# Performance work log

Hardware: AMD Instinct MI355X
Metric: run time of the kernel (lower is better)

## Reference

```python
import jax, jax.numpy as jnp
import numpy as np

B = 64        # number of queries (eg_idx groups)
EPQ = 2048    # edges per query (contiguous blocks, sorted by eg_idx)
E = B * EPQ   # 131072 total edges
D = 128       # n_dims_in; G3 dim = 4*D = 512
N = 50000     # number of visited nodes
K = 256       # max_edges (top-k per query)


def setup_inputs() -> dict:
    key = jax.random.key(0)
    ks = jax.random.split(key, 9)
    scale = np.sqrt(2.0 / (4 * D)).astype(np.float32)
    return {
        "visited_node_score": jax.random.uniform(ks[0], (N,), jnp.float32),
        "visited_node_representation": jax.random.normal(ks[1], (N, D), jnp.float32),
        "rel_emb": jax.random.normal(ks[2], (E, D), jnp.float32),
        "query_src_ts_emb": jax.random.normal(ks[3], (B, D), jnp.float32),
        "query_rel_emb": jax.random.normal(ks[4], (B, D), jnp.float32),
        "Wq": jax.random.normal(ks[5], (4 * D, 4 * D), jnp.float32) * scale,
        "Wk": jax.random.normal(ks[6], (4 * D, 4 * D), jnp.float32) * scale,
        # sorted eg_idx with exactly EPQ edges per query -> regular per-group topk
        "eg_idx": (jnp.arange(E) // EPQ).astype(jnp.int32),
        "node_idx_i": jax.random.randint(ks[7], (E,), 0, N, jnp.int32),
        "node_idx_j": jax.random.randint(ks[8], (E,), 0, N, jnp.int32),
        "k": K,
    }


def segment_softmax(logits, seg, num_segments):
    # numerically-stable softmax over edges sharing the same source node
    m = jax.ops.segment_max(logits, seg, num_segments=num_segments)
    m = jax.lax.stop_gradient(m)
    ex = jnp.exp(logits - m[seg])
    s = jax.ops.segment_sum(ex, seg, num_segments=num_segments)
    return ex / s[seg]


def reference(visited_node_score, visited_node_representation, rel_emb,
              query_src_ts_emb, query_rel_emb, Wq, Wk,
              eg_idx, node_idx_i, node_idx_j, k):
    # gather node / query embeddings per edge (torch index_select)
    hvi = visited_node_representation[node_idx_i]          # [E, D]
    hvj = visited_node_representation[node_idx_j]          # [E, D]
    qs = query_src_ts_emb[eg_idx]                          # [E, D]
    qr = query_rel_emb[eg_idx]                             # [E, D]
    # G3 bilinear: sum(query_proj(cat(left)) * key_proj(cat(right)), -1)
    left = jnp.concatenate([hvi, rel_emb, qs, qr], axis=-1)   # [E, 4D]
    right = jnp.concatenate([hvj, rel_emb, qs, qr], axis=-1)  # [E, 4D]
    logits = jnp.sum((left @ Wq.T) * (right @ Wk.T), axis=-1) # [E]
    # softmax over edges grouped by source node idx (edges[:, -2])
    attn = segment_softmax(logits, node_idx_i, N)              # [E]
    src_score = visited_node_score[node_idx_i]                 # [E]
    target_score = attn * src_score                            # [E]
    # per-query top-k pruning (each query owns a contiguous EPQ block, EPQ > k)
    top_vals, top_idx = jax.lax.top_k(target_score.reshape(B, EPQ), k)
    flat_idx = (top_idx + jnp.arange(B, dtype=top_idx.dtype)[:, None] * EPQ).reshape(-1)
    pruned_attn = attn[flat_idx]                # transition_logits_pruned_softmax
    pruned_src = src_score[flat_idx]            # pruned_src_score
    pruned_tgt = node_idx_j[flat_idx]           # pruned_edges[:, 7]
    # 'sum' node score aggregation: sparse mm == segment_sum of attn * src_score
    updated_node_score = jax.ops.segment_sum(pruned_attn * pruned_src,
                                             pruned_tgt, num_segments=N)
    return updated_node_score
```

## Files before the change

kernel.cpp:

```cpp
#include <hip/hip_runtime.h>
#include <cstddef>

#define EPQ_SHIFT 11
#define KSEL 256

typedef __attribute__((ext_vector_type(8))) short short8v;
typedef __attribute__((ext_vector_type(4))) float float4v;

__device__ __forceinline__ unsigned enc_f(float f) {
  unsigned u = __float_as_uint(f);
  return (u & 0x80000000u) ? ~u : (u | 0x80000000u);
}
__device__ __forceinline__ float dec_f(unsigned k) {
  unsigned u = (k & 0x80000000u) ? (k ^ 0x80000000u) : ~k;
  return __uint_as_float(u);
}
__device__ __forceinline__ unsigned short f2bf(float x) {
  unsigned u = __float_as_uint(x);
  return (unsigned short)((u + 0x7FFFu + ((u >> 16) & 1u)) >> 16);
}

__global__ __launch_bounds__(256) void k1_gemmM(
    const float* __restrict__ Wq, const float* __restrict__ Wk,
    float* __restrict__ M, float* __restrict__ Mt,
    unsigned short* __restrict__ Mh, unsigned short* __restrict__ Ml,
    unsigned short* __restrict__ Mth, unsigned short* __restrict__ Mtl,
    float* __restrict__ outz, float* __restrict__ segsum,
    unsigned* __restrict__ segkey, int N) {
  int tid = threadIdx.x;
  {
    int bid = blockIdx.y * gridDim.x + blockIdx.x;
    for (int idx = bid * 256 + tid; idx < N; idx += 16384) {
      outz[idx] = 0.f;
      segsum[idx] = 0.f;
      segkey[idx] = 0u;
    }
  }
  __shared__ float as[16][64];
  __shared__ float bs[16][64];
  int tx = tid & 15, ty = tid >> 4;
  int c1b = blockIdx.y * 64, c2b = blockIdx.x * 64;
  float acc[4][4] = {};
  for (int k0 = 0; k0 < 512; k0 += 16) {
#pragma unroll
    for (int l = 0; l < 4; ++l) {
      int lin = tid + l * 256;
      int kk = lin >> 6, c = lin & 63;
      as[kk][c] = Wq[(k0 + kk) * 512 + c1b + c];
      bs[kk][c] = Wk[(k0 + kk) * 512 + c2b + c];
    }
    __syncthreads();
#pragma unroll
    for (int kk = 0; kk < 16; ++kk) {
      float a[4], b[4];
#pragma unroll
      for (int m = 0; m < 4; ++m) a[m] = as[kk][ty * 4 + m];
#pragma unroll
      for (int n = 0; n < 4; ++n) b[n] = bs[kk][tx * 4 + n];
#pragma unroll
      for (int m = 0; m < 4; ++m)
#pragma unroll
        for (int n = 0; n < 4; ++n) acc[m][n] += a[m] * b[n];
    }
    __syncthreads();
  }
#pragma unroll
  for (int m = 0; m < 4; ++m)
#pragma unroll
    for (int n = 0; n < 4; ++n) {
      int c1 = c1b + ty * 4 + m, c2 = c2b + tx * 4 + n;
      float v = acc[m][n];
      M[c1 * 512 + c2] = v;
      Mt[c2 * 512 + c1] = v;
      unsigned short h = f2bf(v);
      unsigned short lo = f2bf(v - __uint_as_float((unsigned)h << 16));
      Mh[c1 * 512 + c2] = h;
      Ml[c1 * 512 + c2] = lo;
      Mth[c2 * 512 + c1] = h;
      Mtl[c2 * 512 + c1] = lo;
    }
}

#define STAGE_A_F32(SRC_PTR)                                                 \
  {                                                                          \
    const float* s = (SRC_PTR);                                              \
    float4 v0 = *(const float4*)&s[0];                                       \
    float4 v1 = *(const float4*)&s[4];                                       \
    float4 v2 = *(const float4*)&s[8];                                       \
    float4 v3 = *(const float4*)&s[12];                                      \
    float vv[16] = {v0.x, v0.y, v0.z, v0.w, v1.x, v1.y, v1.z, v1.w,          \
                    v2.x, v2.y, v2.z, v2.w, v3.x, v3.y, v3.z, v3.w};         \
    unsigned hw[8], lw[8];                                                   \
    _Pragma("unroll") for (int j = 0; j < 8; ++j) {                          \
      unsigned short h0 = f2bf(vv[2 * j]);                                   \
      unsigned short h1 = f2bf(vv[2 * j + 1]);                               \
      unsigned short l0 =                                                    \
          f2bf(vv[2 * j] - __uint_as_float((unsigned)h0 << 16));             \
      unsigned short l1 =                                                    \
          f2bf(vv[2 * j + 1] - __uint_as_float((unsigned)h1 << 16));         \
      hw[j] = (unsigned)h0 | ((unsigned)h1 << 16);                           \
      lw[j] = (unsigned)l0 | ((unsigned)l1 << 16);                           \
    }                                                                        \
    int sw = (sn >> 1) & 3;                                                  \
    int g0 = (shalf * 2) ^ sw, g1 = (shalf * 2 + 1) ^ sw;                    \
    *(uint4*)&Ah[sn][g0 * 8] = make_uint4(hw[0], hw[1], hw[2], hw[3]);       \
    *(uint4*)&Ah[sn][g1 * 8] = make_uint4(hw[4], hw[5], hw[6], hw[7]);       \
    *(uint4*)&Al[sn][g0 * 8] = make_uint4(lw[0], lw[1], lw[2], lw[3]);       \
    *(uint4*)&Al[sn][g1 * 8] = make_uint4(lw[4], lw[5], lw[6], lw[7]);       \
  }

#define STAGE_B_BF16(HSRC, LSRC)                                             \
  {                                                                          \
    const unsigned short* sh_ = (HSRC);                                      \
    const unsigned short* sl_ = (LSRC);                                      \
    uint4 q0 = *(const uint4*)&sh_[0];                                       \
    uint4 q1 = *(const uint4*)&sh_[8];                                       \
    uint4 p0 = *(const uint4*)&sl_[0];                                       \
    uint4 p1 = *(const uint4*)&sl_[8];                                       \
    int sw = (sn >> 1) & 3;                                                  \
    int g0 = (shalf * 2) ^ sw, g1 = (shalf * 2 + 1) ^ sw;                    \
    *(uint4*)&Bh[sn][g0 * 8] = q0;                                           \
    *(uint4*)&Bh[sn][g1 * 8] = q1;                                           \
    *(uint4*)&Bl[sn][g0 * 8] = p0;                                           \
    *(uint4*)&Bl[sn][g1 * 8] = p1;                                           \
  }

#define MFMA_CHUNK()                                                         \
  {                                                                          \
    int ln = lane & 15, kq = lane >> 4;                                      \
    short8v ah[4], al[4];                                                    \
    _Pragma("unroll") for (int r = 0; r < 4; ++r) {                          \
      int row = wr2 * 64 + r * 16 + ln;                                      \
      int gg = kq ^ ((row >> 1) & 3);                                        \
      ah[r] = *(const short8v*)&Ah[row][gg * 8];                             \
      al[r] = *(const short8v*)&Al[row][gg * 8];                             \
    }                                                                        \
    _Pragma("unroll") for (int c = 0; c < 4; ++c) {                          \
      int col = wc2 * 64 + c * 16 + ln;                                      \
      int gg = kq ^ ((col >> 1) & 3);                                        \
      short8v bh = *(const short8v*)&Bh[col][gg * 8];                        \
      short8v bl = *(const short8v*)&Bl[col][gg * 8];                        \
      _Pragma("unroll") for (int r = 0; r < 4; ++r) {                        \
        acc[r][c] = __builtin_amdgcn_mfma_f32_16x16x32_bf16(                 \
            ah[r], bh, acc[r][c], 0, 0, 0);                                  \
        acc[r][c] = __builtin_amdgcn_mfma_f32_16x16x32_bf16(                 \
            ah[r], bl, acc[r][c], 0, 0, 0);                                  \
        acc[r][c] = __builtin_amdgcn_mfma_f32_16x16x32_bf16(                 \
            al[r], bh, acc[r][c], 0, 0, 0);                                  \
      }                                                                      \
    }                                                                        \
  }

__global__ __launch_bounds__(256) void k2m_mfma(
    const float* __restrict__ hv, const unsigned short* __restrict__ Mh,
    const unsigned short* __restrict__ Ml, const unsigned short* __restrict__ Mth,
    const unsigned short* __restrict__ Mtl, float* __restrict__ Tj,
    float* __restrict__ I1, int N) {
  __shared__ char pool[32768];
  unsigned short (*Ah)[32] = (unsigned short(*)[32])pool;
  unsigned short (*Al)[32] = (unsigned short(*)[32])(pool + 8192);
  unsigned short (*Bh)[32] = (unsigned short(*)[32])(pool + 16384);
  unsigned short (*Bl)[32] = (unsigned short(*)[32])(pool + 24576);
  float (*ep)[34] = (float(*)[34])pool;

  const int tid = threadIdx.x;
  const int lane = tid & 63;
  const int w = tid >> 6;
  const int wr2 = w >> 1, wc2 = w & 1;
  const int p = blockIdx.x;
  const int n0 = blockIdx.y * 128;
  const unsigned short* bhs = (p == 2) ? Mth : Mh;
  const unsigned short* bls = (p == 2) ? Mtl : Ml;
  const int rowoff = (p == 0) ? 0 : 128;
  float* outp = (p == 0) ? Tj : (p == 1) ? (Tj + 128) : I1;
  const size_t ostride = (p == 2) ? 128 : 256;

  float4v acc[4][4];
#pragma unroll
  for (int r = 0; r < 4; ++r)
#pragma unroll
    for (int c = 0; c < 4; ++c) acc[r][c] = (float4v){0.f, 0.f, 0.f, 0.f};

  const int sn = tid >> 1, shalf = tid & 1;
  for (int ch = 0; ch < 4; ++ch) {
    __syncthreads();
    {
      int gn = n0 + sn;
      gn = gn < N ? gn : N - 1;
      STAGE_A_F32(hv + (size_t)gn * 128 + ch * 32 + shalf * 16);
      size_t boff = (size_t)(rowoff + sn) * 512 + ch * 32 + shalf * 16;
      STAGE_B_BF16(bhs + boff, bls + boff);
    }
    __syncthreads();
    MFMA_CHUNK();
  }

  for (int g = 0; g < 4; ++g) {
    __syncthreads();
    if (wc2 == (g >> 1)) {
      int ln = lane & 15, kq = lane >> 4;
#pragma unroll
      for (int cc = 0; cc < 2; ++cc) {
        int c = (g & 1) * 2 + cc;
#pragma unroll
        for (int r = 0; r < 4; ++r)
#pragma unroll
          for (int reg = 0; reg < 4; ++reg)
            ep[wr2 * 64 + r * 16 + kq * 4 + reg][cc * 16 + ln] = acc[r][c][reg];
      }
    }
    __syncthreads();
    int row = tid >> 1, half = tid & 1;
    int gn = n0 + row;
    if (gn < N) {
#pragma unroll
      for (int j = 0; j < 4; ++j)
        *(float4*)&outp[(size_t)gn * ostride + 32 * g + 16 * half + 4 * j] =
            *(const float4*)&ep[row][16 * half + 4 * j];
    }
  }
}

__global__ __launch_bounds__(256) void k3_query(const float* __restrict__ qsrc,
                                                const float* __restrict__ qrel,
                                                const float* __restrict__ M,
                                                const float* __restrict__ Mt,
                                                float* __restrict__ wv,
                                                float* __restrict__ uv,
                                                float* __restrict__ yv,
                                                float* __restrict__ cb) {
  __shared__ float qcat[256];
  __shared__ float prt[5][256];
  __shared__ float red[128];
  int b = blockIdx.x, tid = threadIdx.x;
  int d = tid & 127, hc = tid >> 7;
  qcat[tid] = (tid < 128) ? qsrc[b * 128 + tid] : qrel[b * 128 + (tid - 128)];
  __syncthreads();
  float w = 0.f, u = 0.f, y = 0.f, t1 = 0.f, t2 = 0.f;
  for (int c = hc * 128; c < hc * 128 + 128; ++c) {
    float q = qcat[c];
    size_t row = (size_t)(256 + c) * 512;
    w += Mt[row + d] * q;
    u += M[row + d] * q;
    y += (Mt[row + 128 + d] + M[row + 128 + d]) * q;
    t1 += M[row + 256 + d] * q;
    t2 += M[row + 384 + d] * q;
  }
  prt[0][tid] = w; prt[1][tid] = u; prt[2][tid] = y;
  prt[3][tid] = t1; prt[4][tid] = t2;
  __syncthreads();
  if (tid < 128) {
    float wc_ = prt[0][d] + prt[0][128 + d];
    float uc = prt[1][d] + prt[1][128 + d];
    float yc = prt[2][d] + prt[2][128 + d];
    float t1c = prt[3][d] + prt[3][128 + d];
    float t2c = prt[4][d] + prt[4][128 + d];
    wv[b * 128 + d] = wc_;
    uv[b * 128 + d] = uc;
    yv[b * 128 + d] = yc;
    red[d] = qcat[d] * t1c + qcat[128 + d] * t2c;
  }
  __syncthreads();
  for (int s = 64; s > 0; s >>= 1) {
    if (tid < s) red[tid] += red[tid + s];
    __syncthreads();
  }
  if (tid == 0) cb[b] = red[0];
}

__global__ __launch_bounds__(256) void k4m_mfma(
    const float* __restrict__ rel, const unsigned short* __restrict__ Mth,
    const unsigned short* __restrict__ Mtl, const float* __restrict__ yv,
    const float* __restrict__ cbp, float* __restrict__ ec) {
  __shared__ char pool[32768];
  unsigned short (*Ah)[32] = (unsigned short(*)[32])pool;
  unsigned short (*Al)[32] = (unsigned short(*)[32])(pool + 8192);
  unsigned short (*Bh)[32] = (unsigned short(*)[32])(pool + 16384);
  unsigned short (*Bl)[32] = (unsigned short(*)[32])(pool + 24576);
  float (*ep)[34] = (float(*)[34])pool;

  const int tid = threadIdx.x;
  const int lane = tid & 63;
  const int w = tid >> 6;
  const int wr2 = w >> 1, wc2 = w & 1;
  const int e0 = blockIdx.x * 128;
  const int b = e0 >> EPQ_SHIFT;

  float4v acc[4][4];
#pragma unroll
  for (int r = 0; r < 4; ++r)
#pragma unroll
    for (int c = 0; c < 4; ++c) acc[r][c] = (float4v){0.f, 0.f, 0.f, 0.f};

  const int sn = tid >> 1, shalf = tid & 1;
  for (int ch = 0; ch < 4; ++ch) {
    __syncthreads();
    {
      STAGE_A_F32(rel + (size_t)(e0 + sn) * 128 + ch * 32 + shalf * 16);
      size_t boff = (size_t)(128 + sn) * 512 + 128 + ch * 32 + shalf * 16;
      STAGE_B_BF16(Mth + boff, Mtl + boff);
    }
    __syncthreads();
    MFMA_CHUNK();
  }

  float part = 0.f;
  const int e_loc = tid >> 1, half = tid & 1;
  for (int g = 0; g < 4; ++g) {
    __syncthreads();
    if (wc2 == (g >> 1)) {
      int ln = lane & 15, kq = lane >> 4;
#pragma unroll
      for (int cc = 0; cc < 2; ++cc) {
        int c = (g & 1) * 2 + cc;
#pragma unroll
        for (int r = 0; r < 4; ++r)
#pragma unroll
          for (int reg = 0; reg < 4; ++reg)
            ep[wr2 * 64 + r * 16 + kq * 4 + reg][cc * 16 + ln] = acc[r][c][reg];
      }
    }
    __syncthreads();
    const float* rsrc = rel + (size_t)(e0 + e_loc) * 128 + 32 * g + 16 * half;
    const float* ysrc = yv + b * 128 + 32 * g + 16 * half;
#pragma unroll
    for (int j = 0; j < 4; ++j) {
      float4 q = *(const float4*)&ep[e_loc][16 * half + 4 * j];
      float4 rr = *(const float4*)&rsrc[4 * j];
      float4 yy = *(const float4*)&ysrc[4 * j];
      part += (q.x + yy.x) * rr.x + (q.y + yy.y) * rr.y +
              (q.z + yy.z) * rr.z + (q.w + yy.w) * rr.w;
    }
  }
  part += __shfl_xor(part, 1, 64);
  if ((tid & 1) == 0) ec[e0 + e_loc] = part + cbp[b];
}

__global__ __launch_bounds__(256) void k5_logits(const float* __restrict__ rel,
                                                 const float* __restrict__ hv,
                                                 const float* __restrict__ Tj,
                                                 const float* __restrict__ I1,
                                                 const float* __restrict__ wv,
                                                 const float* __restrict__ uv,
                                                 const float* __restrict__ ec,
                                                 const int* __restrict__ node_i,
                                                 const int* __restrict__ node_j,
                                                 float* __restrict__ logits,
                                                 unsigned* __restrict__ segkey) {
  __shared__ float wl[128];
  __shared__ float ul[128];
  int tid = threadIdx.x;
  int e0 = blockIdx.x * 16;
  int b = e0 >> EPQ_SHIFT;
  if (tid < 128) wl[tid] = wv[b * 128 + tid];
  else ul[tid - 128] = uv[b * 128 + (tid - 128)];
  __syncthreads();
  int lane = tid & 15, eg = tid >> 4;
  int e = e0 + eg;
  int i = node_i[e], j = node_j[e];
  int c0 = lane * 8;

  float rr[8], hi[8], hj[8], a0[8], a1[8], ii[8];
  *(float4*)&rr[0] = *(const float4*)&rel[(size_t)e * 128 + c0];
  *(float4*)&rr[4] = *(const float4*)&rel[(size_t)e * 128 + c0 + 4];
  *(float4*)&hi[0] = *(const float4*)&hv[(size_t)i * 128 + c0];
  *(float4*)&hi[4] = *(const float4*)&hv[(size_t)i * 128 + c0 + 4];
  *(float4*)&hj[0] = *(const float4*)&hv[(size_t)j * 128 + c0];
  *(float4*)&hj[4] = *(const float4*)&hv[(size_t)j * 128 + c0 + 4];
  *(float4*)&a0[0] = *(const float4*)&Tj[(size_t)j * 256 + c0];
  *(float4*)&a0[4] = *(const float4*)&Tj[(size_t)j * 256 + c0 + 4];
  *(float4*)&a1[0] = *(const float4*)&Tj[(size_t)j * 256 + 128 + c0];
  *(float4*)&a1[4] = *(const float4*)&Tj[(size_t)j * 256 + 128 + c0 + 4];
  *(float4*)&ii[0] = *(const float4*)&I1[(size_t)i * 128 + c0];
  *(float4*)&ii[4] = *(const float4*)&I1[(size_t)i * 128 + c0 + 4];

  float p = 0.f;
#pragma unroll
  for (int k = 0; k < 8; ++k) {
    p += hi[k] * a0[k];
    p += rr[k] * (a1[k] + ii[k]);
    p += hi[k] * wl[c0 + k];
    p += hj[k] * ul[c0 + k];
  }
#pragma unroll
  for (int m = 8; m >= 1; m >>= 1) p += __shfl_xor(p, m, 64);
  if (lane == 0) {
    float lg = p + ec[e];
    logits[e] = lg;
    atomicMax(&segkey[i], enc_f(lg));
  }
}

__global__ void k6_exp(float* __restrict__ exb, const int* __restrict__ node_i,
                       const unsigned* __restrict__ segkey,
                       float* __restrict__ segsum, int E) {
  int e = blockIdx.x * 256 + threadIdx.x;
  if (e >= E) return;
  int i = node_i[e];
  float m = dec_f(segkey[i]);
  float ex = expf(exb[e] - m);
  exb[e] = ex;
  atomicAdd(&segsum[i], ex);
}

__global__ __launch_bounds__(256) void k7_topk(const float* __restrict__ exb,
                                               const int* __restrict__ node_i,
                                               const int* __restrict__ node_j,
                                               const float* __restrict__ segsum,
                                               const float* __restrict__ score,
                                               float* __restrict__ out) {
  __shared__ unsigned vals[2048];
  __shared__ unsigned hist[256];
  __shared__ unsigned sc[256];
  __shared__ unsigned tie_scan[256];
  __shared__ unsigned sel_info[2];
  int q = blockIdx.x, t = threadIdx.x;
  size_t base = (size_t)q * 2048;
#pragma unroll
  for (int l = 0; l < 8; ++l) {
    int el = t * 8 + l;
    int i = node_i[base + el];
    float tgt = exb[base + el] / segsum[i] * score[i];
    vals[el] = __float_as_uint(tgt);
  }
  __syncthreads();
  unsigned prefix = 0, need = KSEL;
  for (int pass = 3; pass >= 0; --pass) {
    hist[t] = 0;
    __syncthreads();
    int sh = pass * 8;
#pragma unroll
    for (int l = 0; l < 8; ++l) {
      unsigned v = vals[t * 8 + l];
      bool match = (pass == 3) || ((v >> (sh + 8)) == (prefix >> (sh + 8)));
      if (match) atomicAdd(&hist[(v >> sh) & 255u], 1u);
    }
    __syncthreads();
    sc[t] = hist[t];
    __syncthreads();
    for (int off = 1; off < 256; off <<= 1) {
      unsigned add = (t + off < 256) ? sc[t + off] : 0u;
      __syncthreads();
      sc[t] += add;
      __syncthreads();
    }
    unsigned above = sc[t] - hist[t];
    if (above < need && need <= sc[t]) {
      sel_info[0] = (unsigned)t;
      sel_info[1] = need - above;
    }
    __syncthreads();
    prefix |= sel_info[0] << sh;
    need = sel_info[1];
    __syncthreads();
  }
  unsigned T = prefix, r = need;
  unsigned lc = 0;
#pragma unroll
  for (int l = 0; l < 8; ++l)
    if (vals[t * 8 + l] == T) lc++;
  tie_scan[t] = lc;
  __syncthreads();
  unsigned own = lc;
  for (int off = 1; off < 256; off <<= 1) {
    unsigned add = (t >= off) ? tie_scan[t - off] : 0u;
    __syncthreads();
    tie_scan[t] += add;
    __syncthreads();
  }
  unsigned excl = tie_scan[t] - own;
  unsigned cnt = 0;
#pragma unroll
  for (int l = 0; l < 8; ++l) {
    int el = t * 8 + l;
    unsigned v = vals[el];
    bool take = false;
    if (v > T) take = true;
    else if (v == T) { if (excl + cnt < r) take = true; cnt++; }
    if (take) {
      int j = node_j[base + el];
      atomicAdd(&out[j], __uint_as_float(v));
    }
  }
}

extern "C" void kernel_launch(void* const* d_in, const int* in_sizes, int n_in,
                              void* d_out, int out_size, void* d_ws, size_t ws_size,
                              hipStream_t stream) {
  const float* score = (const float*)d_in[0];
  const float* hv    = (const float*)d_in[1];
  const float* rel   = (const float*)d_in[2];
  const float* qsrc  = (const float*)d_in[3];
  const float* qrel  = (const float*)d_in[4];
  const float* Wq    = (const float*)d_in[5];
  const float* Wk    = (const float*)d_in[6];
  const int* node_i  = (const int*)d_in[8];
  const int* node_j  = (const int*)d_in[9];

  const int N = in_sizes[0];
  const int B = in_sizes[3] / 128;
  const int E = in_sizes[2] / 128;

  float* ws = (float*)d_ws;
  float* M  = ws;
  float* Mt = M + 262144;
  float* Tj = Mt + 262144;
  float* I1 = Tj + (size_t)N * 256;
  float* wv = I1 + (size_t)N * 128;
  float* uv = wv + (size_t)B * 128;
  float* yv = uv + (size_t)B * 128;
  float* cb = yv + (size_t)B * 128;
  float* ec = cb + B;
  float* exb = ec + E;
  unsigned* segkey = (unsigned*)(exb + E);
  float* segsum = (float*)(segkey + N);
  unsigned short* Mh  = (unsigned short*)(segsum + N);
  unsigned short* Ml  = Mh + 262144;
  unsigned short* Mth = Ml + 262144;
  unsigned short* Mtl = Mth + 262144;
  float* out = (float*)d_out;

  k1_gemmM<<<dim3(8, 8), 256, 0, stream>>>(Wq, Wk, M, Mt, Mh, Ml, Mth, Mtl,
                                           out, segsum, segkey, N);
  k2m_mfma<<<dim3(3, (N + 127) / 128), 256, 0, stream>>>(hv, Mh, Ml, Mth, Mtl,
                                                         Tj, I1, N);
  k3_query<<<B, 256, 0, stream>>>(qsrc, qrel, M, Mt, wv, uv, yv, cb);
  k4m_mfma<<<E / 128, 256, 0, stream>>>(rel, Mth, Mtl, yv, cb, ec);
  k5_logits<<<E / 16, 256, 0, stream>>>(rel, hv, Tj, I1, wv, uv, ec,
                                        node_i, node_j, exb, segkey);
  k6_exp<<<(E + 255) / 256, 256, 0, stream>>>(exb, node_i, segkey, segsum, E);
  k7_topk<<<B, 256, 0, stream>>>(exb, node_i, node_j, segsum, score, out);
}
```

Measured before the change: 237.3 us.

## Fuse three node-projection GEMMs into one kernel reusing staged hv tiles

The node-side MFMA kernel now processes 64-node tiles and loops over all three output projections (Tj halves and I1) inside one block. The hv rows are converted to bf16 hi/lo once and kept in shared memory, so they are not reloaded and resplit for each projection. This trades a smaller tile and fewer blocks (less parallelism, more LDS per block) for reading and converting hv only once. The logits kernel is also split into two launches over half the edges each, which looks neutral or exploratory.

```diff
diff --git a/kernel.cpp b/kernel.cpp
--- a/kernel.cpp
+++ b/kernel.cpp
@@ -151,72 +151,131 @@
     }                                                                        \
   }
 
-__global__ __launch_bounds__(256) void k2m_mfma(
+__global__ __launch_bounds__(256) void k2m3_mfma(
     const float* __restrict__ hv, const unsigned short* __restrict__ Mh,
     const unsigned short* __restrict__ Ml, const unsigned short* __restrict__ Mth,
     const unsigned short* __restrict__ Mtl, float* __restrict__ Tj,
     float* __restrict__ I1, int N) {
-  __shared__ char pool[32768];
-  unsigned short (*Ah)[32] = (unsigned short(*)[32])pool;
-  unsigned short (*Al)[32] = (unsigned short(*)[32])(pool + 8192);
-  unsigned short (*Bh)[32] = (unsigned short(*)[32])(pool + 16384);
-  unsigned short (*Bl)[32] = (unsigned short(*)[32])(pool + 24576);
-  float (*ep)[34] = (float(*)[34])pool;
+  __shared__ char pool[49152];
+  unsigned short (*Ah4)[64][32] = (unsigned short(*)[64][32])pool;
+  unsigned short (*Al4)[64][32] = (unsigned short(*)[64][32])(pool + 16384);
+  unsigned short (*Bh)[32] = (unsigned short(*)[32])(pool + 32768);
+  unsigned short (*Bl)[32] = (unsigned short(*)[32])(pool + 40960);
+  float (*ep)[34] = (float(*)[34])(pool + 32768);
 
   const int tid = threadIdx.x;
   const int lane = tid & 63;
   const int w = tid >> 6;
   const int wr2 = w >> 1, wc2 = w & 1;
-  const int p = blockIdx.x;
-  const int n0 = blockIdx.y * 128;
-  const unsigned short* bhs = (p == 2) ? Mth : Mh;
-  const unsigned short* bls = (p == 2) ? Mtl : Ml;
-  const int rowoff = (p == 0) ? 0 : 128;
-  float* outp = (p == 0) ? Tj : (p == 1) ? (Tj + 128) : I1;
-  const size_t ostride = (p == 2) ? 128 : 256;
-
-  float4v acc[4][4];
-#pragma unroll
-  for (int r = 0; r < 4; ++r)
-#pragma unroll
-    for (int c = 0; c < 4; ++c) acc[r][c] = (float4v){0.f, 0.f, 0.f, 0.f};
-
-  const int sn = tid >> 1, shalf = tid & 1;
-  for (int ch = 0; ch < 4; ++ch) {
-    __syncthreads();
-    {
-      int gn = n0 + sn;
-      gn = gn < N ? gn : N - 1;
-      STAGE_A_F32(hv + (size_t)gn * 128 + ch * 32 + shalf * 16);
-      size_t boff = (size_t)(rowoff + sn) * 512 + ch * 32 + shalf * 16;
-      STAGE_B_BF16(bhs + boff, bls + boff);
-    }
-    __syncthreads();
-    MFMA_CHUNK();
-  }
-
-  for (int g = 0; g < 4; ++g) {
-    __syncthreads();
-    if (wc2 == (g >> 1)) {
-      int ln = lane & 15, kq = lane >> 4;
-#pragma unroll
-      for (int cc = 0; cc < 2; ++cc) {
-        int c = (g & 1) * 2 + cc;
-#pragma unroll
-        for (int r = 0; r < 4; ++r)
-#pragma unroll
-          for (int reg = 0; reg < 4; ++reg)
-            ep[wr2 * 64 + r * 16 + kq * 4 + reg][cc * 16 + ln] = acc[r][c][reg];
+  const int n0 = blockIdx.x * 64;
+
+  {
+    const int n = tid >> 2, q = tid & 3;
+    int gn = n0 + n;
+    gn = gn < N ? gn : N - 1;
+    const int g = q ^ ((n >> 1) & 3);
+#pragma unroll
+    for (int ch = 0; ch < 4; ++ch) {
+      float4 v0 = *(const float4*)&hv[(size_t)gn * 128 + ch * 32 + q * 8];
+      float4 v1 = *(const float4*)&hv[(size_t)gn * 128 + ch * 32 + q * 8 + 4];
+      float vv[8] = {v0.x, v0.y, v0.z, v0.w, v1.x, v1.y, v1.z, v1.w};
+      unsigned hw[4], lw[4];
+#pragma unroll
+      for (int j = 0; j < 4; ++j) {
+        unsigned short h0 = f2bf(vv[2 * j]);
+        unsigned short h1 = f2bf(vv[2 * j + 1]);
+        unsigned short l0 = f2bf(vv[2 * j] - __uint_as_float((unsigned)h0 << 16));
+        unsigned short l1 = f2bf(vv[2 * j + 1] - __uint_as_float((unsigned)h1 << 16));
+        hw[j] = (unsigned)h0 | ((unsigned)h1 << 16);
+        lw[j] = (unsigned)l0 | ((unsigned)l1 << 16);
       }
-    }
-    __syncthreads();
-    int row = tid >> 1, half = tid & 1;
-    int gn = n0 + row;
-    if (gn < N) {
-#pragma unroll
-      for (int j = 0; j < 4; ++j)
-        *(float4*)&outp[(size_t)gn * ostride + 32 * g + 16 * half + 4 * j] =
-            *(const float4*)&ep[row][16 * half + 4 * j];
+      *(uint4*)&Ah4[ch][n][g * 8] = make_uint4(hw[0], hw[1], hw[2], hw[3]);
+      *(uint4*)&Al4[ch][n][g * 8] = make_uint4(lw[0], lw[1], lw[2], lw[3]);
+    }
+  }
+
+  for (int p = 0; p < 3; ++p) {
+    const unsigned short* bhs = (p == 2) ? Mth : Mh;
+    const unsigned short* bls = (p == 2) ? Mtl : Ml;
+    const int borow = (p == 0) ? 0 : 128;
+    float* outp = (p == 0) ? Tj : (p == 1) ? (Tj + 128) : I1;
+    const size_t ostride = (p == 2) ? 128 : 256;
+
+    float4v acc[2][4];
+#pragma unroll
+    for (int r = 0; r < 2; ++r)
+#pragma unroll
+      for (int c = 0; c < 4; ++c) acc[r][c] = (float4v){0.f, 0.f, 0.f, 0.f};
+
+    for (int ch = 0; ch < 4; ++ch) {
+      __syncthreads();
+      {
+        const int d = tid >> 1, half = tid & 1;
+        size_t boff = (size_t)(borow + d) * 512 + ch * 32 + half * 16;
+        uint4 q0 = *(const uint4*)&bhs[boff];
+        uint4 q1 = *(const uint4*)&bhs[boff + 8];
+        uint4 p0 = *(const uint4*)&bls[boff];
+        uint4 p1 = *(const uint4*)&bls[boff + 8];
+        int sw = (d >> 1) & 3;
+        int g0 = (half * 2) ^ sw, g1 = (half * 2 + 1) ^ sw;
+        *(uint4*)&Bh[d][g0 * 8] = q0;
+        *(uint4*)&Bh[d][g1 * 8] = q1;
+        *(uint4*)&Bl[d][g0 * 8] = p0;
+        *(uint4*)&Bl[d][g1 * 8] = p1;
+      }
+      __syncthreads();
+      {
+        int ln = lane & 15, kq = lane >> 4;
+        short8v ah[2], al[2];
+#pragma unroll
+        for (int r = 0; r < 2; ++r) {
+          int row = wr2 * 32 + r * 16 + ln;
+          int gg = kq ^ ((row >> 1) & 3);
+          ah[r] = *(const short8v*)&Ah4[ch][row][gg * 8];
+          al[r] = *(const short8v*)&Al4[ch][row][gg * 8];
+        }
+#pragma unroll
+        for (int c = 0; c < 4; ++c) {
+          int col = wc2 * 64 + c * 16 + ln;
+          int gg = kq ^ ((col >> 1) & 3);
+          short8v bh = *(const short8v*)&Bh[col][gg * 8];
+          short8v bl = *(const short8v*)&Bl[col][gg * 8];
+#pragma unroll
+          for (int r = 0; r < 2; ++r) {
+            acc[r][c] = __builtin_amdgcn_mfma_f32_16x16x32_bf16(ah[r], bh,
+                                                                acc[r][c], 0, 0, 0);
+            acc[r][c] = __builtin_amdgcn_mfma_f32_16x16x32_bf16(ah[r], bl,
+                                                                acc[r][c], 0, 0, 0);
+            acc[r][c] = __builtin_amdgcn_mfma_f32_16x16x32_bf16(al[r], bh,
+                                                                acc[r][c], 0, 0, 0);
+          }
+        }
+      }
+    }
+
+    for (int g = 0; g < 4; ++g) {
+      __syncthreads();
+      if (wc2 == (g >> 1)) {
+        int ln = lane & 15, kq = lane >> 4;
+#pragma unroll
+        for (int cc = 0; cc < 2; ++cc) {
+          int c = (g & 1) * 2 + cc;
+#pragma unroll
+          for (int r = 0; r < 2; ++r)
+#pragma unroll
+            for (int reg = 0; reg < 4; ++reg)
+              ep[wr2 * 32 + r * 16 + kq * 4 + reg][cc * 16 + ln] = acc[r][c][reg];
+        }
+      }
+      __syncthreads();
+      int row = tid >> 2, part = tid & 3;
+      int gn = n0 + row;
+      if (gn < N) {
+        *(float4*)&outp[(size_t)gn * ostride + g * 32 + part * 8] =
+            *(const float4*)&ep[row][part * 8];
+        *(float4*)&outp[(size_t)gn * ostride + g * 32 + part * 8 + 4] =
+            *(const float4*)&ep[row][part * 8 + 4];
+      }
     }
   }
 }
@@ -346,11 +405,12 @@
                                                  const int* __restrict__ node_i,
                                                  const int* __restrict__ node_j,
                                                  float* __restrict__ logits,
-                                                 unsigned* __restrict__ segkey) {
+                                                 unsigned* __restrict__ segkey,
+                                                 int e_base) {
   __shared__ float wl[128];
   __shared__ float ul[128];
   int tid = threadIdx.x;
-  int e0 = blockIdx.x * 16;
+  int e0 = e_base + blockIdx.x * 16;
   int b = e0 >> EPQ_SHIFT;
   if (tid < 128) wl[tid] = wv[b * 128 + tid];
   else ul[tid - 128] = uv[b * 128 + (tid - 128)];
@@ -522,12 +582,13 @@
 
   k1_gemmM<<<dim3(8, 8), 256, 0, stream>>>(Wq, Wk, M, Mt, Mh, Ml, Mth, Mtl,
                                            out, segsum, segkey, N);
-  k2m_mfma<<<dim3(3, (N + 127) / 128), 256, 0, stream>>>(hv, Mh, Ml, Mth, Mtl,
-                                                         Tj, I1, N);
+  k2m3_mfma<<<(N + 63) / 64, 256, 0, stream>>>(hv, Mh, Ml, Mth, Mtl, Tj, I1, N);
   k3_query<<<B, 256, 0, stream>>>(qsrc, qrel, M, Mt, wv, uv, yv, cb);
   k4m_mfma<<<E / 128, 256, 0, stream>>>(rel, Mth, Mtl, yv, cb, ec);
-  k5_logits<<<E / 16, 256, 0, stream>>>(rel, hv, Tj, I1, wv, uv, ec,
-                                        node_i, node_j, exb, segkey);
+  k5_logits<<<E / 32, 256, 0, stream>>>(rel, hv, Tj, I1, wv, uv, ec,
+                                        node_i, node_j, exb, segkey, 0);
+  k5_logits<<<E / 32, 256, 0, stream>>>(rel, hv, Tj, I1, wv, uv, ec,
+                                        node_i, node_j, exb, segkey, E / 2);
   k6_exp<<<(E + 255) / 256, 256, 0, stream>>>(exb, node_i, segkey, segsum, E);
   k7_topk<<<B, 256, 0, stream>>>(exb, node_i, node_j, segsum, score, out);
 }
```

Result: no change. 236.2 us (-0.4%).
